# Performance work log

Hardware: AMD Instinct MI355X
Metric: run time of the kernel (lower is better)

## Reference

```python
import jax, jax.numpy as jnp
import numpy as np

N, E = 10000, 320000
C_IN, C_OUT = 256, 128
EPS = 1e-5


def _p(key, shape, scale=0.02):
    return (jax.random.normal(key, shape, dtype=jnp.float32) * scale)


def setup_inputs() -> dict:
    key = jax.random.key(0)
    ks = jax.random.split(key, 16)
    inp = {
        "x": jax.random.normal(ks[0], (N, C_IN), dtype=jnp.float32),
        "edge_index": jax.random.randint(ks[1], (2, E), 0, N, dtype=jnp.int64),
        # GCNConv weights (stored [in, out] so forward is x @ W)
        "W1": _p(ks[2], (C_IN, C_OUT)), "b1": jnp.zeros((C_OUT,), jnp.float32),
        "W2": _p(ks[3], (C_OUT, C_OUT)), "b2": jnp.zeros((C_OUT,), jnp.float32),
        # LayerNorms
        "ln1_g": jnp.ones((C_OUT,), jnp.float32), "ln1_b": jnp.zeros((C_OUT,), jnp.float32),
        "ln2_g": jnp.ones((C_OUT,), jnp.float32), "ln2_b": jnp.zeros((C_OUT,), jnp.float32),
        # Attention QKV
        "Wq": _p(ks[4], (C_OUT, C_OUT)), "bq": jnp.zeros((C_OUT,), jnp.float32),
        "Wk": _p(ks[5], (C_OUT, C_OUT)), "bk": jnp.zeros((C_OUT,), jnp.float32),
        "Wv": _p(ks[6], (C_OUT, C_OUT)), "bv": jnp.zeros((C_OUT,), jnp.float32),
        # shortcut Linear (in_channels != out_channels)
        "Ws": _p(ks[7], (C_IN, C_OUT)), "bs": jnp.zeros((C_OUT,), jnp.float32),
    }
    return inp


def _gcn_conv(x, W, b, src, dst, n_nodes):
    # PyG GCNConv: h = x W; add self loops; sym-normalized scatter aggregation.
    h = x @ W  # [N, out]
    loop = jnp.arange(n_nodes, dtype=src.dtype)
    s = jnp.concatenate([src, loop])
    d = jnp.concatenate([dst, loop])
    deg = jax.ops.segment_sum(jnp.ones_like(d, dtype=h.dtype), d, num_segments=n_nodes)
    dis = jnp.where(deg > 0, jax.lax.rsqrt(deg), 0.0)  # deg^-1/2
    norm = dis[s] * dis[d]  # [E+N]
    agg = jax.ops.segment_sum(h[s] * norm[:, None], d, num_segments=n_nodes)
    return agg + b


def _layer_norm(x, g, b):
    mu = jnp.mean(x, axis=-1, keepdims=True)
    var = jnp.var(x, axis=-1, keepdims=True)
    return (x - mu) * jax.lax.rsqrt(var + EPS) * g + b


def reference(x, edge_index, W1, b1, W2, b2, ln1_g, ln1_b, ln2_g, ln2_b,
              Wq, bq, Wk, bk, Wv, bv, Ws, bs):
    src, dst = edge_index[0], edge_index[1]
    n = x.shape[0]
    identity = x @ Ws + bs
    out = _gcn_conv(x, W1, b1, src, dst, n)
    out = jax.nn.silu(_layer_norm(out, ln1_g, ln1_b))  # dropout = identity (eval)
    out = _gcn_conv(out, W2, b2, src, dst, n)
    out = _layer_norm(out, ln2_g, ln2_b)
    # dense self-attention over all nodes
    q = out @ Wq + bq
    k = out @ Wk + bk
    v = out @ Wv + bv
    scale = np.sqrt(out.shape[-1]).astype(np.float32)
    attn = jax.nn.softmax(q @ k.T / scale, axis=-1)  # [N, N]
    out = attn @ v + out
    return jax.nn.silu(out + identity)
```

## Files before the change

### kernel.cpp

```cpp
#include <hip/hip_runtime.h>
#include <hip/hip_bf16.h>

typedef unsigned short u16;
typedef unsigned int u32;
typedef __bf16 bf16x8 __attribute__((ext_vector_type(8)));
typedef float f32x4 __attribute__((ext_vector_type(4)));

#define MFMA16(a, b, c) __builtin_amdgcn_mfma_f32_16x16x32_bf16(a, b, c, 0, 0, 0)

static __device__ __forceinline__ u16 f2b(float f) {
  u32 u = __float_as_uint(f);
  return (u16)((u + 0x7FFFu + ((u >> 16) & 1u)) >> 16);
}
static __device__ __forceinline__ float blo(u32 u) { return __uint_as_float(u << 16); }
static __device__ __forceinline__ float bhi(u32 u) { return __uint_as_float(u & 0xffff0000u); }
static __device__ __forceinline__ u32 packtrunc(float a, float b) {
  return (__float_as_uint(a) >> 16) | (__float_as_uint(b) & 0xffff0000u);
}
static __device__ __forceinline__ bf16x8 mk8(u32 a, u32 b, u32 c, u32 d) {
  union { u32 u[4]; bf16x8 v; } t; t.u[0] = a; t.u[1] = b; t.u[2] = c; t.u[3] = d; return t.v;
}

static __device__ __forceinline__ void async_copy16(void* lds, const void* gp) {
  __builtin_amdgcn_global_load_lds(
      (const __attribute__((address_space(1))) unsigned int*)gp,
      (__attribute__((address_space(3))) unsigned int*)lds, 16, 0, 0);
}

__global__ void prep_kernel(const int* __restrict__ dst, int* __restrict__ degi, int E,
                            const float* __restrict__ x, u16* __restrict__ xb, int n4,
                            const float* __restrict__ W1, const float* __restrict__ Ws,
                            const float* __restrict__ W2, const float* __restrict__ Wq,
                            const float* __restrict__ Wk, const float* __restrict__ Wv,
                            u16* __restrict__ wout) {
  int t = blockIdx.x * 256 + threadIdx.x;
  if (t < E) { atomicAdd(&degi[dst[t]], 1); return; }
  int t2 = t - E;
  if (t2 < n4) {
    float4 v = *(const float4*)&x[t2 * 4];
    ushort4 o;
    o.x = f2b(v.x); o.y = f2b(v.y); o.z = f2b(v.z); o.w = f2b(v.w);
    *(ushort4*)&xb[t2 * 4] = o;
    return;
  }
  int u = t2 - n4;
  if (u >= 131072) return;
  const float* src; int K, base, loc;
  if (u < 65536) {
    if (u < 32768) { src = W1; base = 0; } else { src = Ws; base = 32768; }
    loc = u - base; K = 256;
  } else {
    int seg = (u - 65536) >> 14;
    src = (seg == 0) ? W2 : (seg == 1) ? Wq : (seg == 2) ? Wk : Wv;
    base = 65536 + seg * 16384; loc = u & 16383; K = 128;
  }
  int k = loc >> 7, c = loc & 127;
  wout[base + c * K + k] = f2b(src[loc]);
}

__global__ void dis_start_kernel(const int* __restrict__ degi, float* __restrict__ d,
                                 int* __restrict__ startb, int* __restrict__ counter, int N) {
  int i = blockIdx.x * 256 + threadIdx.x;
  int lane = threadIdx.x & 63;
  int dg = (i < N) ? degi[i] : 0;
  if (i < N) d[i] = rsqrtf((float)dg + 1.0f);
  int x = dg;
#pragma unroll
  for (int ofs = 1; ofs < 64; ofs <<= 1) {
    int y = __shfl_up(x, ofs, 64);
    if (lane >= ofs) x += y;
  }
  int waveTotal = __shfl(x, 63, 64);
  int base = 0;
  if (lane == 63) base = atomicAdd(counter, waveTotal);
  base = __shfl(base, 63, 64);
  if (i < N) startb[i] = base + x - dg;
}

__global__ void fill_kernel(const int* __restrict__ src, const int* __restrict__ dst,
                            const int* __restrict__ startb, int* __restrict__ cursor,
                            int* __restrict__ adj, int E) {
  int e = blockIdx.x * 256 + threadIdx.x;
  if (e < E) {
    int d = dst[e];
    int p = atomicAdd(&cursor[d], 1);
    adj[startb[d] + p] = src[e];
  }
}

__global__ __launch_bounds__(64) void bgemm_dual(
    const u16* __restrict__ A, const u16* __restrict__ Wa, const u16* __restrict__ Wb,
    const float* __restrict__ bsb, u16* __restrict__ outa, float* __restrict__ outb, int M)
{
  int lane = threadIdx.x;
  int col = lane & 15, quad = lane >> 4;
  int row0 = blockIdx.x * 16;
  int cb = blockIdx.y * 64;
  int ar = row0 + col; if (ar > M - 1) ar = M - 1;
  const u16* ap = A + (size_t)ar * 256 + quad * 8;
  f32x4 Oa[4], Ob[4];
#pragma unroll
  for (int i = 0; i < 4; i++) {
    Oa[i][0] = 0.f; Oa[i][1] = 0.f; Oa[i][2] = 0.f; Oa[i][3] = 0.f;
    Ob[i] = Oa[i];
  }
#pragma unroll
  for (int k0 = 0; k0 < 256; k0 += 32) {
    bf16x8 aA = *(const bf16x8*)(ap + k0);
#pragma unroll
    for (int nb = 0; nb < 4; nb++) {
      size_t wofs = (size_t)(cb + nb * 16 + col) * 256 + k0 + quad * 8;
      Oa[nb] = MFMA16(aA, *(const bf16x8*)(Wa + wofs), Oa[nb]);
      Ob[nb] = MFMA16(aA, *(const bf16x8*)(Wb + wofs), Ob[nb]);
    }
  }
#pragma unroll
  for (int nb = 0; nb < 4; nb++) {
    int ch = cb + nb * 16 + col;
    float bv = bsb[ch];
#pragma unroll
    for (int r = 0; r < 4; r++) {
      int row = row0 + quad * 4 + r;
      if (row >= M) continue;
      outa[(size_t)row * 128 + ch] = f2b(Oa[nb][r]);
      outb[(size_t)row * 128 + ch] = Ob[nb][r] + bv;
    }
  }
}

static __device__ __forceinline__ void gather_rows_to_lds(
    const u16* __restrict__ h, const float* __restrict__ dis,
    const int* __restrict__ adj, const int* __restrict__ startb, const int* __restrict__ degi,
    const float* __restrict__ bias, const float* __restrict__ g, const float* __restrict__ beta,
    u16* Ao, float* curOut, int row0, int N, int do_silu)
{
  int w = threadIdx.x >> 6, lane = threadIdx.x & 63;
  int c2 = lane * 2;
  for (int rr = 0; rr < 4; rr++) {
    int rl = w * 4 + rr;
    int row = row0 + rl;
    float o0 = 0.f, o1 = 0.f;
    if (row < N) {
      int st = startb[row], dg = degi[row];
      float v0 = 0.f, v1 = 0.f;
      for (int base = 0; base < dg; base += 64) {
        int nb = min(64, dg - base);
        int myadj = 0; float mydis = 0.f;
        if (lane < nb) { myadj = adj[st + base + lane]; mydis = dis[myadj]; }
        int jj = 0;
        for (; jj + 8 <= nb; jj += 8) {
          int s0 = __shfl(myadj, jj),     s1 = __shfl(myadj, jj + 1);
          int s2 = __shfl(myadj, jj + 2), s3 = __shfl(myadj, jj + 3);
          int s4 = __shfl(myadj, jj + 4), s5 = __shfl(myadj, jj + 5);
          int s6 = __shfl(myadj, jj + 6), s7 = __shfl(myadj, jj + 7);
          float w0 = __shfl(mydis, jj),     w1 = __shfl(mydis, jj + 1);
          float w2 = __shfl(mydis, jj + 2), w3 = __shfl(mydis, jj + 3);
          float w4 = __shfl(mydis, jj + 4), w5 = __shfl(mydis, jj + 5);
          float w6 = __shfl(mydis, jj + 6), w7 = __shfl(mydis, jj + 7);
          u32 a0 = *(const u32*)&h[(size_t)s0 * 128 + c2];
          u32 a1 = *(const u32*)&h[(size_t)s1 * 128 + c2];
          u32 a2 = *(const u32*)&h[(size_t)s2 * 128 + c2];
          u32 a3 = *(const u32*)&h[(size_t)s3 * 128 + c2];
          u32 a4 = *(const u32*)&h[(size_t)s4 * 128 + c2];
          u32 a5 = *(const u32*)&h[(size_t)s5 * 128 + c2];
          u32 a6 = *(const u32*)&h[(size_t)s6 * 128 + c2];
          u32 a7 = *(const u32*)&h[(size_t)s7 * 128 + c2];
          v0 += w0 * blo(a0); v1 += w0 * bhi(a0);
          v0 += w1 * blo(a1); v1 += w1 * bhi(a1);
          v0 += w2 * blo(a2); v1 += w2 * bhi(a2);
          v0 += w3 * blo(a3); v1 += w3 * bhi(a3);
          v0 += w4 * blo(a4); v1 += w4 * bhi(a4);
          v0 += w5 * blo(a5); v1 += w5 * bhi(a5);
          v0 += w6 * blo(a6); v1 += w6 * bhi(a6);
          v0 += w7 * blo(a7); v1 += w7 * bhi(a7);
        }
        for (; jj < nb; jj++) {
          int s = __shfl(myadj, jj);
          float wv = __shfl(mydis, jj);
          u32 a = *(const u32*)&h[(size_t)s * 128 + c2];
          v0 += wv * blo(a); v1 += wv * bhi(a);
        }
      }
      float dd = dis[row];
      u32 aself = *(const u32*)&h[(size_t)row * 128 + c2];
      v0 = (v0 + dd * blo(aself)) * dd + bias[c2];
      v1 = (v1 + dd * bhi(aself)) * dd + bias[c2 + 1];
      float s = v0 + v1;
#pragma unroll
      for (int d = 32; d > 0; d >>= 1) s += __shfl_xor(s, d, 64);
      float mu = s * (1.0f / 128.0f);
      float d0 = v0 - mu, d1 = v1 - mu;
      float q = d0 * d0 + d1 * d1;
#pragma unroll
      for (int d = 32; d > 0; d >>= 1) q += __shfl_xor(q, d, 64);
      float rstd = rsqrtf(q * (1.0f / 128.0f) + 1e-5f);
      o0 = d0 * rstd * g[c2]     + beta[c2];
      o1 = d1 * rstd * g[c2 + 1] + beta[c2 + 1];
      if (do_silu) {
        o0 = o0 / (1.f + __expf(-o0));
        o1 = o1 / (1.f + __expf(-o1));
      }
      if (curOut) *(float2*)&curOut[(size_t)row * 128 + c2] = make_float2(o0, o1);
    }
    *(u32*)&Ao[rl * 136 + c2] = (u32)f2b(o0) | ((u32)f2b(o1) << 16);
  }
}

__global__ __launch_bounds__(256) void gather_gemm1(
    const u16* __restrict__ h, const float* __restrict__ dis,
    const int* __restrict__ adj, const int* __restrict__ startb, const int* __restrict__ degi,
    const float* __restrict__ b1, const float* __restrict__ g1, const float* __restrict__ be1,
    const u16* __restrict__ W2t, u16* __restrict__ h2, int N)
{
  __shared__ __align__(16) u16 Ao[16 * 136];
  int row0 = blockIdx.x * 16;
  gather_rows_to_lds(h, dis, adj, startb, degi, b1, g1, be1, Ao, nullptr, row0, N, 1);
  __syncthreads();
  int lane = threadIdx.x & 63;
  int w = threadIdx.x >> 6;
  int col = lane & 15, quad = lane >> 4;
  int nb0 = w * 2;
  f32x4 acc[2];
#pragma unroll
  for (int t = 0; t < 2; t++) { acc[t][0] = 0.f; acc[t][1] = 0.f; acc[t][2] = 0.f; acc[t][3] = 0.f; }
#pragma unroll
  for (int ks = 0; ks < 4; ks++) {
    bf16x8 aA = *(const bf16x8*)&Ao[col * 136 + ks * 32 + quad * 8];
#pragma unroll
    for (int t = 0; t < 2; t++) {
      const u16* bp = W2t + (size_t)((nb0 + t) * 16 + col) * 128 + ks * 32 + quad * 8;
      acc[t] = MFMA16(aA, *(const bf16x8*)bp, acc[t]);
    }
  }
#pragma unroll
  for (int t = 0; t < 2; t++) {
    int ch = (nb0 + t) * 16 + col;
#pragma unroll
    for (int r = 0; r < 4; r++) {
      int row = row0 + quad * 4 + r;
      if (row < N) h2[(size_t)row * 128 + ch] = f2b(acc[t][r]);
    }
  }
}

__global__ __launch_bounds__(256) void gather_gemm_qkv(
    const u16* __restrict__ h2, const float* __restrict__ dis,
    const int* __restrict__ adj, const int* __restrict__ startb, const int* __restrict__ degi,
    const float* __restrict__ b2, const float* __restrict__ g2, const float* __restrict__ be2,
    const u16* __restrict__ Wqt, const u16* __restrict__ Wkt, const u16* __restrict__ Wvt,
    const float* __restrict__ bq, const float* __restrict__ bk, const float* __restrict__ bv,
    float* __restrict__ cur, u16* __restrict__ q_out, u16* __restrict__ k_out,
    u16* __restrict__ v_out, int N, int NP, float qscale)
{
  __shared__ __align__(16) u16 Ao[16 * 136];
  int row0 = blockIdx.x * 16;
  gather_rows_to_lds(h2, dis, adj, startb, degi, b2, g2, be2, Ao, cur, row0, N, 0);
  __syncthreads();
  int lane = threadIdx.x & 63;
  int w = threadIdx.x >> 6;
  int col = lane & 15, quad = lane >> 4;
  int nb0 = w * 2;
  f32x4 Oq[2], Ok[2], Ov[2];
#pragma unroll
  for (int t = 0; t < 2; t++) {
    Oq[t][0] = 0.f; Oq[t][1] = 0.f; Oq[t][2] = 0.f; Oq[t][3] = 0.f;
    Ok[t] = Oq[t]; Ov[t] = Oq[t];
  }
#pragma unroll
  for (int ks = 0; ks < 4; ks++) {
    bf16x8 aA = *(const bf16x8*)&Ao[col * 136 + ks * 32 + quad * 8];
#pragma unroll
    for (int t = 0; t < 2; t++) {
      size_t wofs = (size_t)((nb0 + t) * 16 + col) * 128 + ks * 32 + quad * 8;
      Oq[t] = MFMA16(aA, *(const bf16x8*)(Wqt + wofs), Oq[t]);
      Ok[t] = MFMA16(aA, *(const bf16x8*)(Wkt + wofs), Ok[t]);
      Ov[t] = MFMA16(aA, *(const bf16x8*)(Wvt + wofs), Ov[t]);
    }
  }
#pragma unroll
  for (int t = 0; t < 2; t++) {
    int ch = (nb0 + t) * 16 + col;
    float bqv = bq[ch], bkv = bk[ch], bvv = bv[ch];
#pragma unroll
    for (int r = 0; r < 4; r++) {
      int row = row0 + quad * 4 + r;
      if (row >= N) continue;
      q_out[(size_t)row * 128 + ch] = f2b((Oq[t][r] + bqv) * qscale);
      k_out[(size_t)row * 128 + ch] = f2b(Ok[t][r] + bkv);
      v_out[(size_t)ch * NP + row] = f2b(Ov[t][r] + bvv);
    }
  }
}

__global__ __launch_bounds__(256, 3) void flash_part(
    const u16* __restrict__ qb, const u16* __restrict__ kb, const u16* __restrict__ vt,
    u16* __restrict__ Opart, float* __restrict__ lpart,
    int N, int NP, int NPB, int CHUNK)
{
  __shared__ __align__(16) u16 Kl[2][32 * 128];
  __shared__ __align__(16) u16 Vl[2][128 * 32];
  int tid = threadIdx.x;
  int w = tid >> 6, lane = tid & 63;
  int col = lane & 15, quad = lane >> 4;
  int h8 = col & 7;
  int ks = blockIdx.y;
  int kstart = ks * CHUNK;
  int qbase = blockIdx.x * 128 + w * 32;

  bf16x8 aQ[2][4];
#pragma unroll
  for (int rg = 0; rg < 2; rg++) {
    int qr = qbase + rg * 16 + col; if (qr > N - 1) qr = N - 1;
    const u16* qp = qb + (size_t)qr * 128 + quad * 8;
    aQ[rg][0] = *(const bf16x8*)(qp);
    aQ[rg][1] = *(const bf16x8*)(qp + 32);
    aQ[rg][2] = *(const bf16x8*)(qp + 64);
    aQ[rg][3] = *(const bf16x8*)(qp + 96);
  }

  f32x4 O[2][8];
#pragma unroll
  for (int rg = 0; rg < 2; rg++)
#pragma unroll
    for (int i = 0; i < 8; i++) { O[rg][i][0] = 0.f; O[rg][i][1] = 0.f; O[rg][i][2] = 0.f; O[rg][i][3] = 0.f; }
  float lr0 = 0.f, lr1 = 0.f;

  int l16 = lane >> 4, c16 = lane & 15;
  int vch = lane >> 2, vc4 = lane & 3;

  int idxA = (((quad & 1) * 2 + 0) * 16 + col) * 4;
  int idxB = (((quad & 1) * 2 + 1) * 16 + col) * 4;
  bool hiKg = (quad >= 2);

  auto stage = [&](int buf, int k0) {
#pragma unroll
    for (int i = 0; i < 2; i++) {
      int rl = w * 8 + i * 4 + l16;
      int cg = c16 ^ (rl & 7);
      async_copy16(&Kl[buf][(w * 8 + i * 4) * 128], kb + (size_t)(k0 + rl) * 128 + cg * 8);
    }
#pragma unroll
    for (int i = 0; i < 2; i++) {
      int ch = w * 32 + i * 16 + vch;
      int cg = vc4 ^ ((ch >> 1) & 3);
      async_copy16(&Vl[buf][(w * 32 + i * 16) * 32], vt + (size_t)ch * NP + k0 + cg * 8);
    }
  };

  int KT = (min(CHUNK, NP - kstart)) >> 5;
  stage(0, kstart);

  for (int kt = 0; kt < KT; kt++) {
    int buf = kt & 1;
    int k0 = kstart + (kt << 5);
    asm volatile("s_waitcnt vmcnt(0)\n\ts_barrier" ::: "memory");
    if (kt + 1 < KT) stage(buf ^ 1, k0 + 32);

    const u16* Kb = &Kl[buf][0];
    const u16* Vb = &Vl[buf][0];

    f32x4 sT[2][2];
#pragma unroll
    for (int kg = 0; kg < 2; kg++) {
      const u16* kr = Kb + (kg * 16 + col) * 128;
      bf16x8 kf0 = *(const bf16x8*)(kr + (((0 + quad) ^ h8) << 3));
      bf16x8 kf1 = *(const bf16x8*)(kr + (((4 + quad) ^ h8) << 3));
      bf16x8 kf2 = *(const bf16x8*)(kr + (((8 + quad) ^ h8) << 3));
      bf16x8 kf3 = *(const bf16x8*)(kr + (((12 + quad) ^ h8) << 3));
      f32x4 s0; s0[0] = 0.f; s0[1] = 0.f; s0[2] = 0.f; s0[3] = 0.f;
      f32x4 s1 = s0;
      s0 = MFMA16(kf0, aQ[0][0], s0); s1 = MFMA16(kf0, aQ[1][0], s1);
      s0 = MFMA16(kf1, aQ[0][1], s0); s1 = MFMA16(kf1, aQ[1][1], s1);
      s0 = MFMA16(kf2, aQ[0][2], s0); s1 = MFMA16(kf2, aQ[1][2], s1);
      s0 = MFMA16(kf3, aQ[0][3], s0); s1 = MFMA16(kf3, aQ[1][3], s1);
      sT[kg][0] = s0; sT[kg][1] = s1;
    }
    if (k0 + 32 > N) {
#pragma unroll
      for (int kg = 0; kg < 2; kg++) {
        int kbase = k0 + kg * 16 + quad * 4;
#pragma unroll
        for (int r = 0; r < 4; r++) {
          if (kbase + r >= N) { sT[kg][0][r] = -1e30f; sT[kg][1][r] = -1e30f; }
        }
      }
    }
    u32 plo[2][2], phi[2][2];
#pragma unroll
    for (int kg = 0; kg < 2; kg++) {
      float p00 = __expf(sT[kg][0][0]), p01 = __expf(sT[kg][0][1]);
      float p02 = __expf(sT[kg][0][2]), p03 = __expf(sT[kg][0][3]);
      float p10 = __expf(sT[kg][1][0]), p11 = __expf(sT[kg][1][1]);
      float p12 = __expf(sT[kg][1][2]), p13 = __expf(sT[kg][1][3]);
      lr0 += p00 + p01 + p02 + p03;
      lr1 += p10 + p11 + p12 + p13;
      plo[kg][0] = packtrunc(p00, p01); phi[kg][0] = packtrunc(p02, p03);
      plo[kg][1] = packtrunc(p10, p11); phi[kg][1] = packtrunc(p12, p13);
    }
    bf16x8 bP[2];
#pragma unroll
    for (int rg = 0; rg < 2; rg++) {
      int loA0 = __builtin_amdgcn_ds_bpermute(idxA, (int)plo[0][rg]);
      int loA1 = __builtin_amdgcn_ds_bpermute(idxA, (int)plo[1][rg]);
      int hiA0 = __builtin_amdgcn_ds_bpermute(idxA, (int)phi[0][rg]);
      int hiA1 = __builtin_amdgcn_ds_bpermute(idxA, (int)phi[1][rg]);
      int loB0 = __builtin_amdgcn_ds_bpermute(idxB, (int)plo[0][rg]);
      int loB1 = __builtin_amdgcn_ds_bpermute(idxB, (int)plo[1][rg]);
      int hiB0 = __builtin_amdgcn_ds_bpermute(idxB, (int)phi[0][rg]);
      int hiB1 = __builtin_amdgcn_ds_bpermute(idxB, (int)phi[1][rg]);
      u32 j01 = hiKg ? (u32)loA1 : (u32)loA0;
      u32 j23 = hiKg ? (u32)hiA1 : (u32)hiA0;
      u32 j45 = hiKg ? (u32)loB1 : (u32)loB0;
      u32 j67 = hiKg ? (u32)hiB1 : (u32)hiB0;
      bP[rg] = mk8(j01, j23, j45, j67);
    }
#pragma unroll
    for (int nb = 0; nb < 8; nb++) {
      int ch = nb * 16 + col;
      const u16* vr = Vb + ch * 32;
      bf16x8 vf = *(const bf16x8*)(vr + ((quad ^ ((ch >> 1) & 3)) << 3));
      O[0][nb] = MFMA16(vf, bP[0], O[0][nb]);
      O[1][nb] = MFMA16(vf, bP[1], O[1][nb]);
    }
  }

  lr0 += __shfl_xor(lr0, 16, 64); lr0 += __shfl_xor(lr0, 32, 64);
  lr1 += __shfl_xor(lr1, 16, 64); lr1 += __shfl_xor(lr1, 32, 64);
  if (lane < 16) {
    lpart[(size_t)ks * NPB + qbase + lane] = lr0;
    lpart[(size_t)ks * NPB + qbase + 16 + lane] = lr1;
  }
#pragma unroll
  for (int rg = 0; rg < 2; rg++) {
    int row = qbase + rg * 16 + col;
    u16* dstrow = Opart + ((size_t)ks * NPB + row) * 128 + quad * 4;
#pragma unroll
    for (int nb = 0; nb < 8; nb++) {
      u32 w01 = (u32)f2b(O[rg][nb][0]) | ((u32)f2b(O[rg][nb][1]) << 16);
      u32 w23 = (u32)f2b(O[rg][nb][2]) | ((u32)f2b(O[rg][nb][3]) << 16);
      *(uint2*)(dstrow + nb * 16) = make_uint2(w01, w23);
    }
  }
}

__global__ __launch_bounds__(256) void attn_combine(
    const u16* __restrict__ Opart, const float* __restrict__ lpart,
    const float* __restrict__ out2, const float* __restrict__ ident, float* __restrict__ out,
    int N, int NPB, int S)
{
  int row = blockIdx.x * 4 + (threadIdx.x >> 6);
  int c2 = (threadIdx.x & 63) * 2;
  if (row >= N) return;
  float num0 = 0.f, num1 = 0.f, den = 0.f;
  for (int u = 0; u < S; u++) {
    u32 b = *(const u32*)&Opart[((size_t)u * NPB + row) * 128 + c2];
    num0 += blo(b); num1 += bhi(b);
    den += lpart[(size_t)u * NPB + row];
  }
  size_t idx = (size_t)row * 128 + c2;
  float rinv = 1.0f / den;
  float2 o2 = *(const float2*)&out2[idx];
  float2 id = *(const float2*)&ident[idx];
  float v0 = num0 * rinv + o2.x + id.x;
  float v1 = num1 * rinv + o2.y + id.y;
  v0 = v0 / (1.f + __expf(-v0));
  v1 = v1 / (1.f + __expf(-v1));
  *(float2*)&out[idx] = make_float2(v0, v1);
}

extern "C" void kernel_launch(void* const* d_in, const int* in_sizes, int n_in,
                              void* d_out, int out_size, void* d_ws, size_t ws_size,
                              hipStream_t stream) {
  const float* x   = (const float*)d_in[0];
  const int*   ei  = (const int*)d_in[1];
  const float* W1  = (const float*)d_in[2];
  const float* b1  = (const float*)d_in[3];
  const float* W2  = (const float*)d_in[4];
  const float* b2  = (const float*)d_in[5];
  const float* g1  = (const float*)d_in[6];
  const float* be1 = (const float*)d_in[7];
  const float* g2  = (const float*)d_in[8];
  const float* be2 = (const float*)d_in[9];
  const float* Wq  = (const float*)d_in[10];
  const float* bq  = (const float*)d_in[11];
  const float* Wk  = (const float*)d_in[12];
  const float* bk  = (const float*)d_in[13];
  const float* Wv  = (const float*)d_in[14];
  const float* bv  = (const float*)d_in[15];
  const float* Wsw = (const float*)d_in[16];
  const float* bs  = (const float*)d_in[17];

  const int CIN = 256, C = 128;
  int N = in_sizes[0] / CIN;
  int E = in_sizes[1] / 2;
  int NP = (N + 63) & ~63;
  int NPB = (N + 127) & ~127;
  const int* src = ei;
  const int* dstp = ei + E;

  const int S = 8;
  int tiles = NP / 64;
  int CHUNK = ((tiles + S - 1) / S) * 64;

  char* w = (char*)d_ws;
  size_t off = 0;
  auto alloc = [&](size_t bytes) -> void* {
    void* p = w + off;
    off = (off + bytes + 255) & ~(size_t)255;
    return p;
  };
  int*   degi   = (int*)alloc((size_t)N * 4);
  int*   cursor = (int*)alloc((size_t)N * 4);
  int*   counter= (int*)alloc(256);
  size_t zlen   = off;
  float* disb   = (float*)alloc((size_t)N * 4);
  int*   startb = (int*)alloc((size_t)N * 4);
  int*   adj    = (int*)alloc((size_t)E * 4);
  u16*   h      = (u16*)alloc((size_t)N * C * 2);
  u16*   h2     = (u16*)alloc((size_t)N * C * 2);
  float* ident  = (float*)alloc((size_t)N * C * 4);
  float* cur    = (float*)alloc((size_t)N * C * 4);
  u16*   xb     = (u16*)alloc((size_t)N * CIN * 2);
  u16*   wt     = (u16*)alloc((size_t)131072 * 2);
  u16*   qbb    = (u16*)alloc((size_t)N * C * 2);
  u16*   kbb    = (u16*)alloc((size_t)NP * C * 2);
  u16*   vt     = (u16*)alloc((size_t)C * NP * 2);
  u16*   Opart  = (u16*)alloc((size_t)S * NPB * C * 2);
  float* lpart  = (float*)alloc((size_t)S * NPB * 4);

  u16* wt1 = wt;
  u16* wts = wt + 32768;
  u16* wt2 = wt + 65536;
  u16* wtq = wt + 81920;
  u16* wtk = wt + 98304;
  u16* wtv = wt + 114688;

  hipMemsetAsync(degi, 0, zlen, stream);

  int n4 = N * CIN / 4;
  int ptot = E + n4 + 131072;
  prep_kernel<<<(ptot + 255) / 256, 256, 0, stream>>>(dstp, degi, E, x, xb, n4,
                                                      W1, Wsw, W2, Wq, Wk, Wv, wt);
  int gN = (N + 255) / 256, gE = (E + 255) / 256;
  dis_start_kernel<<<gN, 256, 0, stream>>>(degi, disb, startb, counter, N);
  fill_kernel<<<gE, 256, 0, stream>>>(src, dstp, startb, cursor, adj, E);

  dim3 gbg((N + 15) / 16, 2);
  bgemm_dual<<<gbg, 64, 0, stream>>>(xb, wt1, wts, bs, h, ident, N);

  int gRows = (N + 15) / 16;
  gather_gemm1<<<gRows, 256, 0, stream>>>(h, disb, adj, startb, degi, b1, g1, be1, wt2, h2, N);

  const float qscale = 0.08838834764831845f;
  gather_gemm_qkv<<<gRows, 256, 0, stream>>>(h2, disb, adj, startb, degi, b2, g2, be2,
                                             wtq, wtk, wtv, bq, bk, bv,
                                             cur, qbb, kbb, vt, N, NP, qscale);

  dim3 fg(NPB / 128, S);
  flash_part<<<fg, 256, 0, stream>>>(qbb, kbb, vt, Opart, lpart, N, NP, NPB, CHUNK);
  attn_combine<<<(N + 3) / 4, 256, 0, stream>>>(Opart, lpart, cur, ident,
                                                (float*)d_out, N, NPB, S);
}
```

Measured before the change: 294.0 us.

## Merge CSR fill with input GEMM and use one wave per gathered row

New measurement: 286.1 us. -2.7%, faster.

```diff
diff --git a/kernel.cpp b/kernel.cpp
--- a/kernel.cpp
+++ b/kernel.cpp
@@ -77,25 +77,27 @@
   if (i < N) startb[i] = base + x - dg;
 }
 
-__global__ void fill_kernel(const int* __restrict__ src, const int* __restrict__ dst,
-                            const int* __restrict__ startb, int* __restrict__ cursor,
-                            int* __restrict__ adj, int E) {
-  int e = blockIdx.x * 256 + threadIdx.x;
-  if (e < E) {
-    int d = dst[e];
-    int p = atomicAdd(&cursor[d], 1);
-    adj[startb[d] + p] = src[e];
-  }
-}
-
-__global__ __launch_bounds__(64) void bgemm_dual(
+__global__ __launch_bounds__(256) void mid_kernel(
+    const int* __restrict__ src, const int* __restrict__ dstp, const int* __restrict__ startb,
+    int* __restrict__ cursor, int* __restrict__ adj, int E, int Gg,
     const u16* __restrict__ A, const u16* __restrict__ Wa, const u16* __restrict__ Wb,
     const float* __restrict__ bsb, u16* __restrict__ outa, float* __restrict__ outb, int M)
 {
-  int lane = threadIdx.x;
+  if ((int)blockIdx.x >= Gg) {
+    int e = (blockIdx.x - Gg) * 256 + threadIdx.x;
+    if (e < E) {
+      int d = dstp[e];
+      int p = atomicAdd(&cursor[d], 1);
+      adj[startb[d] + p] = src[e];
+    }
+    return;
+  }
+  int wv = threadIdx.x >> 6;
+  int lane = threadIdx.x & 63;
   int col = lane & 15, quad = lane >> 4;
-  int row0 = blockIdx.x * 16;
-  int cb = blockIdx.y * 64;
+  int row0 = (blockIdx.x * 2 + (wv >> 1)) * 16;
+  if (row0 >= M) return;
+  int cb = (wv & 1) * 64;
   int ar = row0 + col; if (ar > M - 1) ar = M - 1;
   const u16* ap = A + (size_t)ar * 256 + quad * 8;
   f32x4 Oa[4], Ob[4];
@@ -128,166 +130,169 @@
   }
 }
 
-static __device__ __forceinline__ void gather_rows_to_lds(
+static __device__ __forceinline__ void gather_one_row(
     const u16* __restrict__ h, const float* __restrict__ dis,
     const int* __restrict__ adj, const int* __restrict__ startb, const int* __restrict__ degi,
     const float* __restrict__ bias, const float* __restrict__ g, const float* __restrict__ beta,
-    u16* Ao, float* curOut, int row0, int N, int do_silu)
+    u16* AoRow, float* curOut, int row, int N, int do_silu)
 {
-  int w = threadIdx.x >> 6, lane = threadIdx.x & 63;
+  int lane = threadIdx.x & 63;
   int c2 = lane * 2;
-  for (int rr = 0; rr < 4; rr++) {
-    int rl = w * 4 + rr;
-    int row = row0 + rl;
-    float o0 = 0.f, o1 = 0.f;
-    if (row < N) {
-      int st = startb[row], dg = degi[row];
-      float v0 = 0.f, v1 = 0.f;
-      for (int base = 0; base < dg; base += 64) {
-        int nb = min(64, dg - base);
-        int myadj = 0; float mydis = 0.f;
-        if (lane < nb) { myadj = adj[st + base + lane]; mydis = dis[myadj]; }
-        int jj = 0;
-        for (; jj + 8 <= nb; jj += 8) {
-          int s0 = __shfl(myadj, jj),     s1 = __shfl(myadj, jj + 1);
-          int s2 = __shfl(myadj, jj + 2), s3 = __shfl(myadj, jj + 3);
-          int s4 = __shfl(myadj, jj + 4), s5 = __shfl(myadj, jj + 5);
-          int s6 = __shfl(myadj, jj + 6), s7 = __shfl(myadj, jj + 7);
-          float w0 = __shfl(mydis, jj),     w1 = __shfl(mydis, jj + 1);
-          float w2 = __shfl(mydis, jj + 2), w3 = __shfl(mydis, jj + 3);
-          float w4 = __shfl(mydis, jj + 4), w5 = __shfl(mydis, jj + 5);
-          float w6 = __shfl(mydis, jj + 6), w7 = __shfl(mydis, jj + 7);
-          u32 a0 = *(const u32*)&h[(size_t)s0 * 128 + c2];
-          u32 a1 = *(const u32*)&h[(size_t)s1 * 128 + c2];
-          u32 a2 = *(const u32*)&h[(size_t)s2 * 128 + c2];
-          u32 a3 = *(const u32*)&h[(size_t)s3 * 128 + c2];
-          u32 a4 = *(const u32*)&h[(size_t)s4 * 128 + c2];
-          u32 a5 = *(const u32*)&h[(size_t)s5 * 128 + c2];
-          u32 a6 = *(const u32*)&h[(size_t)s6 * 128 + c2];
-          u32 a7 = *(const u32*)&h[(size_t)s7 * 128 + c2];
-          v0 += w0 * blo(a0); v1 += w0 * bhi(a0);
-          v0 += w1 * blo(a1); v1 += w1 * bhi(a1);
-          v0 += w2 * blo(a2); v1 += w2 * bhi(a2);
-          v0 += w3 * blo(a3); v1 += w3 * bhi(a3);
-          v0 += w4 * blo(a4); v1 += w4 * bhi(a4);
-          v0 += w5 * blo(a5); v1 += w5 * bhi(a5);
-          v0 += w6 * blo(a6); v1 += w6 * bhi(a6);
-          v0 += w7 * blo(a7); v1 += w7 * bhi(a7);
-        }
-        for (; jj < nb; jj++) {
-          int s = __shfl(myadj, jj);
-          float wv = __shfl(mydis, jj);
-          u32 a = *(const u32*)&h[(size_t)s * 128 + c2];
-          v0 += wv * blo(a); v1 += wv * bhi(a);
-        }
+  float o0 = 0.f, o1 = 0.f;
+  if (row < N) {
+    int st = startb[row], dg = degi[row];
+    float v0 = 0.f, v1 = 0.f;
+    for (int base = 0; base < dg; base += 64) {
+      int nb = min(64, dg - base);
+      int myadj = 0; float mydis = 0.f;
+      if (lane < nb) { myadj = adj[st + base + lane]; mydis = dis[myadj]; }
+      int jj = 0;
+      for (; jj + 8 <= nb; jj += 8) {
+        int s0 = __shfl(myadj, jj),     s1 = __shfl(myadj, jj + 1);
+        int s2 = __shfl(myadj, jj + 2), s3 = __shfl(myadj, jj + 3);
+        int s4 = __shfl(myadj, jj + 4), s5 = __shfl(myadj, jj + 5);
+        int s6 = __shfl(myadj, jj + 6), s7 = __shfl(myadj, jj + 7);
+        float w0 = __shfl(mydis, jj),     w1 = __shfl(mydis, jj + 1);
+        float w2 = __shfl(mydis, jj + 2), w3 = __shfl(mydis, jj + 3);
+        float w4 = __shfl(mydis, jj + 4), w5 = __shfl(mydis, jj + 5);
+        float w6 = __shfl(mydis, jj + 6), w7 = __shfl(mydis, jj + 7);
+        u32 a0 = *(const u32*)&h[(size_t)s0 * 128 + c2];
+        u32 a1 = *(const u32*)&h[(size_t)s1 * 128 + c2];
+        u32 a2 = *(const u32*)&h[(size_t)s2 * 128 + c2];
+        u32 a3 = *(const u32*)&h[(size_t)s3 * 128 + c2];
+        u32 a4 = *(const u32*)&h[(size_t)s4 * 128 + c2];
+        u32 a5 = *(const u32*)&h[(size_t)s5 * 128 + c2];
+        u32 a6 = *(const u32*)&h[(size_t)s6 * 128 + c2];
+        u32 a7 = *(const u32*)&h[(size_t)s7 * 128 + c2];
+        v0 += w0 * blo(a0); v1 += w0 * bhi(a0);
+        v0 += w1 * blo(a1); v1 += w1 * bhi(a1);
+        v0 += w2 * blo(a2); v1 += w2 * bhi(a2);
+        v0 += w3 * blo(a3); v1 += w3 * bhi(a3);
+        v0 += w4 * blo(a4); v1 += w4 * bhi(a4);
+        v0 += w5 * blo(a5); v1 += w5 * bhi(a5);
+        v0 += w6 * blo(a6); v1 += w6 * bhi(a6);
+        v0 += w7 * blo(a7); v1 += w7 * bhi(a7);
       }
-      float dd = dis[row];
-      u32 aself = *(const u32*)&h[(size_t)row * 128 + c2];
-      v0 = (v0 + dd * blo(aself)) * dd + bias[c2];
-      v1 = (v1 + dd * bhi(aself)) * dd + bias[c2 + 1];
-      float s = v0 + v1;
-#pragma unroll
-      for (int d = 32; d > 0; d >>= 1) s += __shfl_xor(s, d, 64);
-      float mu = s * (1.0f / 128.0f);
-      float d0 = v0 - mu, d1 = v1 - mu;
-      float q = d0 * d0 + d1 * d1;
-#pragma unroll
-      for (int d = 32; d > 0; d >>= 1) q += __shfl_xor(q, d, 64);
-      float rstd = rsqrtf(q * (1.0f / 128.0f) + 1e-5f);
-      o0 = d0 * rstd * g[c2]     + beta[c2];
-      o1 = d1 * rstd * g[c2 + 1] + beta[c2 + 1];
-      if (do_silu) {
-        o0 = o0 / (1.f + __expf(-o0));
-        o1 = o1 / (1.f + __expf(-o1));
+      for (; jj < nb; jj++) {
+        int s = __shfl(myadj, jj);
+        float wv = __shfl(mydis, jj);
+        u32 a = *(const u32*)&h[(size_t)s * 128 + c2];
+        v0 += wv * blo(a); v1 += wv * bhi(a);
       }
-      if (curOut) *(float2*)&curOut[(size_t)row * 128 + c2] = make_float2(o0, o1);
-    }
-    *(u32*)&Ao[rl * 136 + c2] = (u32)f2b(o0) | ((u32)f2b(o1) << 16);
-  }
-}
-
-__global__ __launch_bounds__(256) void gather_gemm1(
+    }
+    float dd = dis[row];
+    u32 aself = *(const u32*)&h[(size_t)row * 128 + c2];
+    v0 = (v0 + dd * blo(aself)) * dd + bias[c2];
+    v1 = (v1 + dd * bhi(aself)) * dd + bias[c2 + 1];
+    float s = v0 + v1;
+#pragma unroll
+    for (int d = 32; d > 0; d >>= 1) s += __shfl_xor(s, d, 64);
+    float mu = s * (1.0f / 128.0f);
+    float d0 = v0 - mu, d1 = v1 - mu;
+    float q = d0 * d0 + d1 * d1;
+#pragma unroll
+    for (int d = 32; d > 0; d >>= 1) q += __shfl_xor(q, d, 64);
+    float rstd = rsqrtf(q * (1.0f / 128.0f) + 1e-5f);
+    o0 = d0 * rstd * g[c2]     + beta[c2];
+    o1 = d1 * rstd * g[c2 + 1] + beta[c2 + 1];
+    if (do_silu) {
+      o0 = o0 / (1.f + __expf(-o0));
+      o1 = o1 / (1.f + __expf(-o1));
+    }
+    if (curOut) *(float2*)&curOut[(size_t)row * 128 + c2] = make_float2(o0, o1);
+  }
+  *(u32*)&AoRow[c2] = (u32)f2b(o0) | ((u32)f2b(o1) << 16);
+}
+
+__global__ __launch_bounds__(1024) void gather_gemm1(
     const u16* __restrict__ h, const float* __restrict__ dis,
     const int* __restrict__ adj, const int* __restrict__ startb, const int* __restrict__ degi,
     const float* __restrict__ b1, const float* __restrict__ g1, const float* __restrict__ be1,
     const u16* __restrict__ W2t, u16* __restrict__ h2, int N)
 {
   __shared__ __align__(16) u16 Ao[16 * 136];
+  int wv = threadIdx.x >> 6;
   int row0 = blockIdx.x * 16;
-  gather_rows_to_lds(h, dis, adj, startb, degi, b1, g1, be1, Ao, nullptr, row0, N, 1);
+  gather_one_row(h, dis, adj, startb, degi, b1, g1, be1, &Ao[wv * 136], nullptr,
+                 row0 + wv, N, 1);
   __syncthreads();
+  if (wv >= 8) return;
   int lane = threadIdx.x & 63;
-  int w = threadIdx.x >> 6;
   int col = lane & 15, quad = lane >> 4;
-  int nb0 = w * 2;
-  f32x4 acc[2];
-#pragma unroll
-  for (int t = 0; t < 2; t++) { acc[t][0] = 0.f; acc[t][1] = 0.f; acc[t][2] = 0.f; acc[t][3] = 0.f; }
+  f32x4 acc; acc[0] = 0.f; acc[1] = 0.f; acc[2] = 0.f; acc[3] = 0.f;
 #pragma unroll
   for (int ks = 0; ks < 4; ks++) {
     bf16x8 aA = *(const bf16x8*)&Ao[col * 136 + ks * 32 + quad * 8];
-#pragma unroll
-    for (int t = 0; t < 2; t++) {
-      const u16* bp = W2t + (size_t)((nb0 + t) * 16 + col) * 128 + ks * 32 + quad * 8;
-      acc[t] = MFMA16(aA, *(const bf16x8*)bp, acc[t]);
-    }
-  }
-#pragma unroll
-  for (int t = 0; t < 2; t++) {
-    int ch = (nb0 + t) * 16 + col;
-#pragma unroll
-    for (int r = 0; r < 4; r++) {
-      int row = row0 + quad * 4 + r;
-      if (row < N) h2[(size_t)row * 128 + ch] = f2b(acc[t][r]);
-    }
-  }
-}
-
-__global__ __launch_bounds__(256) void gather_gemm_qkv(
+    const u16* bp = W2t + (size_t)(wv * 16 + col) * 128 + ks * 32 + quad * 8;
+    acc = MFMA16(aA, *(const bf16x8*)bp, acc);
+  }
+  int ch = wv * 16 + col;
+#pragma unroll
+  for (int r = 0; r < 4; r++) {
+    int row = row0 + quad * 4 + r;
+    if (row < N) h2[(size_t)row * 128 + ch] = f2b(acc[r]);
+  }
+}
+
+__global__ __launch_bounds__(1024) void gather_gemm_qkv(
     const u16* __restrict__ h2, const float* __restrict__ dis,
     const int* __restrict__ adj, const int* __restrict__ startb, const int* __restrict__ degi,
     const float* __restrict__ b2, const float* __restrict__ g2, const float* __restrict__ be2,
     const u16* __restrict__ Wqt, const u16* __restrict__ Wkt, const u16* __restrict__ Wvt,
-    const float* __restrict__ bq, const float* __restrict__ bk, const float* __restrict__ bv,
+    const float* __restrict__ bq, const float* __restrict__ bk, const float* __restrict__ bvb,
     float* __restrict__ cur, u16* __restrict__ q_out, u16* __restrict__ k_out,
     u16* __restrict__ v_out, int N, int NP, float qscale)
 {
   __shared__ __align__(16) u16 Ao[16 * 136];
+  int wv = threadIdx.x >> 6;
   int row0 = blockIdx.x * 16;
-  gather_rows_to_lds(h2, dis, adj, startb, degi, b2, g2, be2, Ao, cur, row0, N, 0);
+  gather_one_row(h2, dis, adj, startb, degi, b2, g2, be2, &Ao[wv * 136], cur,
+                 row0 + wv, N, 0);
   __syncthreads();
   int lane = threadIdx.x & 63;
-  int w = threadIdx.x >> 6;
   int col = lane & 15, quad = lane >> 4;
-  int nb0 = w * 2;
-  f32x4 Oq[2], Ok[2], Ov[2];
-#pragma unroll
-  for (int t = 0; t < 2; t++) {
-    Oq[t][0] = 0.f; Oq[t][1] = 0.f; Oq[t][2] = 0.f; Oq[t][3] = 0.f;
-    Ok[t] = Oq[t]; Ov[t] = Oq[t];
-  }
-#pragma unroll
-  for (int ks = 0; ks < 4; ks++) {
-    bf16x8 aA = *(const bf16x8*)&Ao[col * 136 + ks * 32 + quad * 8];
-#pragma unroll
-    for (int t = 0; t < 2; t++) {
-      size_t wofs = (size_t)((nb0 + t) * 16 + col) * 128 + ks * 32 + quad * 8;
-      Oq[t] = MFMA16(aA, *(const bf16x8*)(Wqt + wofs), Oq[t]);
-      Ok[t] = MFMA16(aA, *(const bf16x8*)(Wkt + wofs), Ok[t]);
-      Ov[t] = MFMA16(aA, *(const bf16x8*)(Wvt + wofs), Ov[t]);
-    }
-  }
-#pragma unroll
-  for (int t = 0; t < 2; t++) {
-    int ch = (nb0 + t) * 16 + col;
-    float bqv = bq[ch], bkv = bk[ch], bvv = bv[ch];
+  {
+    const u16* Wt = (wv < 8) ? Wqt : Wkt;
+    const float* bb = (wv < 8) ? bq : bk;
+    int cb = (wv & 7) * 16;
+    f32x4 acc; acc[0] = 0.f; acc[1] = 0.f; acc[2] = 0.f; acc[3] = 0.f;
+#pragma unroll
+    for (int ks = 0; ks < 4; ks++) {
+      bf16x8 aA = *(const bf16x8*)&Ao[col * 136 + ks * 32 + quad * 8];
+      const u16* bp = Wt + (size_t)(cb + col) * 128 + ks * 32 + quad * 8;
+      acc = MFMA16(aA, *(const bf16x8*)bp, acc);
+    }
+    int ch = cb + col;
+    float bv = bb[ch];
+    if (wv < 8) {
+#pragma unroll
+      for (int r = 0; r < 4; r++) {
+        int row = row0 + quad * 4 + r;
+        if (row < N) q_out[(size_t)row * 128 + ch] = f2b((acc[r] + bv) * qscale);
+      }
+    } else {
+#pragma unroll
+      for (int r = 0; r < 4; r++) {
+        int row = row0 + quad * 4 + r;
+        if (row < N) k_out[(size_t)row * 128 + ch] = f2b(acc[r] + bv);
+      }
+    }
+  }
+  if (wv < 8) {
+    int cb = wv * 16;
+    f32x4 acc; acc[0] = 0.f; acc[1] = 0.f; acc[2] = 0.f; acc[3] = 0.f;
+#pragma unroll
+    for (int ks = 0; ks < 4; ks++) {
+      bf16x8 aA = *(const bf16x8*)&Ao[col * 136 + ks * 32 + quad * 8];
+      const u16* bp = Wvt + (size_t)(cb + col) * 128 + ks * 32 + quad * 8;
+      acc = MFMA16(aA, *(const bf16x8*)bp, acc);
+    }
+    int ch = cb + col;
+    float bv = bvb[ch];
 #pragma unroll
     for (int r = 0; r < 4; r++) {
       int row = row0 + quad * 4 + r;
-      if (row >= N) continue;
-      q_out[(size_t)row * 128 + ch] = f2b((Oq[t][r] + bqv) * qscale);
-      k_out[(size_t)row * 128 + ch] = f2b(Ok[t][r] + bkv);
-      v_out[(size_t)ch * NP + row] = f2b(Ov[t][r] + bvv);
+      if (row < N) v_out[(size_t)ch * NP + row] = f2b(acc[r] + bv);
     }
   }
 }
@@ -541,20 +546,23 @@
   int ptot = E + n4 + 131072;
   prep_kernel<<<(ptot + 255) / 256, 256, 0, stream>>>(dstp, degi, E, x, xb, n4,
                                                       W1, Wsw, W2, Wq, Wk, Wv, wt);
-  int gN = (N + 255) / 256, gE = (E + 255) / 256;
+  int gN = (N + 255) / 256;
   dis_start_kernel<<<gN, 256, 0, stream>>>(degi, disb, startb, counter, N);
-  fill_kernel<<<gE, 256, 0, stream>>>(src, dstp, startb, cursor, adj, E);
-
-  dim3 gbg((N + 15) / 16, 2);
-  bgemm_dual<<<gbg, 64, 0, stream>>>(xb, wt1, wts, bs, h, ident, N);
+
+  int rowtiles = (N + 15) / 16;
+  int Gg = (rowtiles + 1) / 2;
+  int gE = (E + 255) / 256;
+  mid_kernel<<<Gg + gE, 256, 0, stream>>>(src, dstp, startb, cursor, adj, E, Gg,
+                                          xb, wt1, wts, bs, h, ident, N);
 
   int gRows = (N + 15) / 16;
-  gather_gemm1<<<gRows, 256, 0, stream>>>(h, disb, adj, startb, degi, b1, g1, be1, wt2, h2, N);
+  gather_gemm1<<<gRows, 1024, 0, stream>>>(h, disb, adj, startb, degi, b1, g1, be1,
+                                           wt2, h2, N);
 
   const float qscale = 0.08838834764831845f;
-  gather_gemm_qkv<<<gRows, 256, 0, stream>>>(h2, disb, adj, startb, degi, b2, g2, be2,
-                                             wtq, wtk, wtv, bq, bk, bv,
-                                             cur, qbb, kbb, vt, N, NP, qscale);
+  gather_gemm_qkv<<<gRows, 1024, 0, stream>>>(h2, disb, adj, startb, degi, b2, g2, be2,
+                                              wtq, wtk, wtv, bq, bk, bv,
+                                              cur, qbb, kbb, vt, N, NP, qscale);
 
   dim3 fg(NPB / 128, S);
   flash_part<<<fg, 256, 0, stream>>>(qbb, kbb, vt, Opart, lpart, N, NP, NPB, CHUNK);
```
